# Kernel tuning notes

Measured on AMD Instinct MI355X. Metric: run time of the kernel, lower is better.

The kernel has to match this reference:

```python
import jax, jax.numpy as jnp
import numpy as np

B, CIN, H, W = 16, 256, 56, 56
D, HEADS, KS, PAD, STRIDE, M = 256, 8, 3, 1, 1, 4
K = KS * KS
N = D // HEADS
# relative_indices: sum of window coords, flattened row-major, values in [0, 2*KS-2]
REL = (np.arange(KS)[:, None] + np.arange(KS)[None, :]).reshape(-1)


def setup_inputs() -> dict:
    key = jax.random.key(0)
    ks = jax.random.split(key, 7)
    return {
        "x": jax.random.normal(ks[0], (B, CIN, H, W), jnp.float32),
        "q": jax.random.normal(ks[1], (B, D, 1), jnp.float32),
        "Wk": jax.random.normal(ks[2], (D, CIN), jnp.float32) * 0.05,
        "Wv": jax.random.normal(ks[3], (D, CIN), jnp.float32) * 0.05,
        "pos_emb": jax.random.normal(ks[4], (1, 2 * KS - 1), jnp.float32),
        "Wlin": jax.random.normal(ks[5], (1, M), jnp.float32),
        "Wproj": jax.random.normal(ks[6], (D, D), jnp.float32) * 0.05,
    }


def _unfold(t):
    # torch nn.Unfold: (B,C,H,W) -> (B, C*K, L); patches feature dim ordered (C, kh, kw)
    p = jax.lax.conv_general_dilated_patches(
        t, (KS, KS), (STRIDE, STRIDE), [(PAD, PAD), (PAD, PAD)])
    b, _, ho, wo = p.shape
    return p.reshape(b, -1, ho * wo), ho, wo


def reference(x, q, Wk, Wv, pos_emb, Wlin, Wproj):
    b = x.shape[0]
    k = jnp.einsum('oc,bchw->bohw', Wk, x)  # 1x1 conv, no bias
    v = jnp.einsum('oc,bchw->bohw', Wv, x)
    ku, ho, wo = _unfold(k)
    vu, _, _ = _unfold(v)
    L = ho * wo
    ku = ku.reshape(b, HEADS, N, K, L)  # (b, h, n, k, l)
    vu = vu.reshape(b, HEADS, N, K, L)
    qh = q.reshape(b, HEADS, N)  # learned per-batch query, d=1 squeezed
    attn = jnp.einsum('bhn,bhnkl->bhlk', qh, ku)  # (b,h,l,K)
    attn = attn + pos_emb[0, REL]  # relative position bias, shape (K,)
    attn = jax.nn.softmax(attn, axis=-1)
    # repeat d(=1) -> m identical rows then Linear(m,1,no bias): equals scale by sum(Wlin)
    attn = attn * jnp.sum(Wlin)
    out = jnp.einsum('bhlk,bhnkl->bhnl', attn, vu)  # (b,h,n,l)
    out = out.reshape(b, D, ho, wo)  # fold with kernel 1 == reshape
    return jnp.einsum('oc,bchw->bohw', Wproj, out)  # 1x1 proj conv
```

## Files before the change

### kernel.cpp

```cpp
#include <hip/hip_runtime.h>

#define B_     16
#define D_     256
#define HEADS_ 8
#define N_     32
#define H_     56
#define W_     56
#define L_     3136
#define LDB    40
#define LDX    66

typedef short short8 __attribute__((ext_vector_type(8)));
typedef float f32x4  __attribute__((ext_vector_type(4)));

__device__ __forceinline__ unsigned short f2bf(float f) {
    union { float f; unsigned u; } c; c.f = f;
    unsigned u = c.u;
    u += 0x7fffu + ((u >> 16) & 1u);
    return (unsigned short)(u >> 16);
}

__global__ __launch_bounds__(256) void convert_w_kernel(
    const float* __restrict__ w0, const float* __restrict__ w1,
    const float* __restrict__ w2, unsigned short* __restrict__ o0,
    unsigned short* __restrict__ o1, unsigned short* __restrict__ o2)
{
    const float* src; unsigned short* dst;
    if (blockIdx.y == 0)      { src = w0; dst = o0; }
    else if (blockIdx.y == 1) { src = w1; dst = o1; }
    else                      { src = w2; dst = o2; }
    const int i = (blockIdx.x * 256 + threadIdx.x) * 4;
    float4 v = *(const float4*)(src + i);
    uint2 o;
    o.x = (unsigned)f2bf(v.x) | ((unsigned)f2bf(v.y) << 16);
    o.y = (unsigned)f2bf(v.z) | ((unsigned)f2bf(v.w) << 16);
    *(uint2*)(dst + i) = o;
}

__global__ __launch_bounds__(256, 2) void gemm_kv_mfma(
    const float* __restrict__ x, const unsigned short* __restrict__ Wkb,
    const unsigned short* __restrict__ Wvb, const float* __restrict__ q,
    unsigned short* __restrict__ Vo, float* __restrict__ S)
{
    __shared__ float Xs[32][LDX];

    const int bb = blockIdx.z;
    const int l0 = blockIdx.x * 64;
    const int t  = threadIdx.x;
    const int w    = t >> 6;
    const int lane = t & 63;
    const int col  = lane & 15;
    const int quad = lane >> 4;

    f32x4 accK[4][4], accV[4][4];
#pragma unroll
    for (int mi = 0; mi < 4; ++mi)
#pragma unroll
        for (int ni = 0; ni < 4; ++ni) {
            accK[mi][ni] = (f32x4){0.f, 0.f, 0.f, 0.f};
            accV[mi][ni] = (f32x4){0.f, 0.f, 0.f, 0.f};
        }

    const int xc = t >> 3;
    const int xl = (t & 7) * 8;
    const float* xrow = x + ((size_t)bb * D_ + xc) * L_ + l0 + xl;

    const unsigned short* wk0 = Wkb + (size_t)(w * 64 + col) * D_ + quad * 8;
    const unsigned short* wv0 = Wvb + (size_t)(w * 64 + col) * D_ + quad * 8;

    for (int kt = 0; kt < 8; ++kt) {
        const int c0 = kt * 32;
        const float* xp = xrow + (size_t)c0 * L_;
        float4 x0 = *(const float4*)xp;
        float4 x1 = *(const float4*)(xp + 4);
        short8 ak[4], av[4];
#pragma unroll
        for (int mi = 0; mi < 4; ++mi) {
            ak[mi] = *(const short8*)(wk0 + (size_t)mi * 16 * D_ + c0);
            av[mi] = *(const short8*)(wv0 + (size_t)mi * 16 * D_ + c0);
        }

        __syncthreads();
        *(float2*)&Xs[xc][xl + 0] = make_float2(x0.x, x0.y);
        *(float2*)&Xs[xc][xl + 2] = make_float2(x0.z, x0.w);
        *(float2*)&Xs[xc][xl + 4] = make_float2(x1.x, x1.y);
        *(float2*)&Xs[xc][xl + 6] = make_float2(x1.z, x1.w);
        __syncthreads();

        short8 bfr[4];
#pragma unroll
        for (int ni = 0; ni < 4; ++ni)
#pragma unroll
            for (int j = 0; j < 8; ++j)
                bfr[ni][j] = (short)f2bf(Xs[quad * 8 + j][ni * 16 + col]);

#pragma unroll
        for (int mi = 0; mi < 4; ++mi)
#pragma unroll
            for (int ni = 0; ni < 4; ++ni) {
                accK[mi][ni] = __builtin_amdgcn_mfma_f32_16x16x32_bf16(ak[mi], bfr[ni], accK[mi][ni], 0, 0, 0);
                accV[mi][ni] = __builtin_amdgcn_mfma_f32_16x16x32_bf16(av[mi], bfr[ni], accV[mi][ni], 0, 0, 0);
            }
    }

#pragma unroll
    for (int mi = 0; mi < 4; ++mi) {
        const int hh = w * 2 + (mi >> 1);
        const int dn = (mi & 1) * 16 + quad * 4;
#pragma unroll
        for (int ni = 0; ni < 4; ++ni) {
            unsigned short pk[4];
#pragma unroll
            for (int r = 0; r < 4; ++r) pk[r] = f2bf(accV[mi][ni][r]);
            const int l = l0 + ni * 16 + col;
            *(uint2*)(Vo + ((((size_t)(bb * HEADS_ + hh)) * L_ + l) << 5) + dn) =
                *(const uint2*)pk;
        }
    }

    float qv[4][4];
#pragma unroll
    for (int mi = 0; mi < 4; ++mi)
#pragma unroll
        for (int r = 0; r < 4; ++r)
            qv[mi][r] = q[bb * D_ + w * 64 + mi * 16 + quad * 4 + r];

#pragma unroll
    for (int ni = 0; ni < 4; ++ni) {
        float s0 = 0.f, s1 = 0.f;
#pragma unroll
        for (int r = 0; r < 4; ++r) {
            s0 = fmaf(qv[0][r], accK[0][ni][r], s0);
            s0 = fmaf(qv[1][r], accK[1][ni][r], s0);
            s1 = fmaf(qv[2][r], accK[2][ni][r], s1);
            s1 = fmaf(qv[3][r], accK[3][ni][r], s1);
        }
        s0 += __shfl_xor(s0, 16, 64);
        s0 += __shfl_xor(s0, 32, 64);
        s1 += __shfl_xor(s1, 16, 64);
        s1 += __shfl_xor(s1, 32, 64);
        if (lane < 16) {
            const int l = l0 + ni * 16 + col;
            S[(size_t)(bb * HEADS_ + w * 2) * L_ + l]     = s0;
            S[(size_t)(bb * HEADS_ + w * 2 + 1) * L_ + l] = s1;
        }
    }
}

__global__ __launch_bounds__(256) void attend_kernel(
    const float* __restrict__ S, const unsigned short* __restrict__ Vo,
    const float* __restrict__ pos_emb, const float* __restrict__ Wlin,
    unsigned short* __restrict__ Om)
{
    __shared__ unsigned short Vs[10][58][8];
    __shared__ float Ss[10][58];

    const int band = blockIdx.x;
    const int half = blockIdx.y;
    const int bh   = blockIdx.z;
    const int y0   = band * 8;
    const int t    = threadIdx.x;

    const float* Sb = S + (size_t)bh * L_;
    for (int j = t; j < 580; j += 256) {
        const int row = j / 58, c = j - row * 58;
        const int gr = y0 - 1 + row, gc = c - 1;
        const bool in = (gr >= 0 && gr < H_ && gc >= 0 && gc < W_);
        Ss[row][c] = in ? Sb[gr * W_ + gc] : 0.f;
        uint4 vv = make_uint4(0u, 0u, 0u, 0u);
        if (in)
            vv = *(const uint4*)(Vo + (((size_t)bh * L_ + gr * W_ + gc) << 5) + half * 8);
        *(uint4*)&Vs[row][c][0] = vv;
    }
    __syncthreads();

    const float scale = Wlin[0] + Wlin[1] + Wlin[2] + Wlin[3];
    const float pe0 = pos_emb[0], pe1 = pos_emb[1], pe2 = pos_emb[2];
    const float pe3 = pos_emb[3], pe4 = pos_emb[4];
    const float bias[9] = {pe0, pe1, pe2, pe1, pe2, pe3, pe2, pe3, pe4};

    for (int p = t; p < 448; p += 256) {
        const int yl = p / 56, xx = p - yl * 56;
        const int lr = yl + 1, lc = xx + 1;

        float lg[9], m = -1e30f;
#pragma unroll
        for (int dy = 0; dy < 3; ++dy)
#pragma unroll
            for (int dx = 0; dx < 3; ++dx) {
                const int k = dy * 3 + dx;
                lg[k] = Ss[lr - 1 + dy][lc - 1 + dx] + bias[k];
                m = fmaxf(m, lg[k]);
            }
        float ssum = 0.f;
#pragma unroll
        for (int k = 0; k < 9; ++k) { lg[k] = __expf(lg[k] - m); ssum += lg[k]; }
        const float inv = scale / ssum;

        float om[8] = {0.f, 0.f, 0.f, 0.f, 0.f, 0.f, 0.f, 0.f};
#pragma unroll
        for (int dy = 0; dy < 3; ++dy)
#pragma unroll
            for (int dx = 0; dx < 3; ++dx) {
                const float wk = lg[dy * 3 + dx] * inv;
                const uint4 v = *(const uint4*)&Vs[lr - 1 + dy][lc - 1 + dx][0];
                const unsigned* u = (const unsigned*)&v;
#pragma unroll
                for (int i = 0; i < 4; ++i) {
                    union { unsigned uu; float f; } lo, hi;
                    lo.uu = u[i] << 16;
                    hi.uu = u[i] & 0xffff0000u;
                    om[2 * i]     = fmaf(wk, lo.f, om[2 * i]);
                    om[2 * i + 1] = fmaf(wk, hi.f, om[2 * i + 1]);
                }
            }

        unsigned short ob[8];
#pragma unroll
        for (int i = 0; i < 8; ++i) ob[i] = f2bf(om[i]);
        const int l = (y0 + yl) * W_ + xx;
        *(uint4*)(Om + (((size_t)bh * L_ + l) << 5) + half * 8) = *(const uint4*)ob;
    }
}

__global__ __launch_bounds__(256, 2) void gemm_proj_mfma(
    const unsigned short* __restrict__ Om, const unsigned short* __restrict__ Wpb,
    float* __restrict__ Out)
{
    __shared__ unsigned short Bs[64][LDB];

    const int bb = blockIdx.z;
    const int l0 = blockIdx.x * 64;
    const int t  = threadIdx.x;
    const int w    = t >> 6;
    const int lane = t & 63;
    const int col  = lane & 15;
    const int quad = lane >> 4;

    f32x4 acc[4][4];
#pragma unroll
    for (int mi = 0; mi < 4; ++mi)
#pragma unroll
        for (int ni = 0; ni < 4; ++ni) acc[mi][ni] = (f32x4){0.f, 0.f, 0.f, 0.f};

    const int srow = t >> 2;
    const int skc  = (t & 3) * 8;
    const unsigned short* wp0 = Wpb + (size_t)(w * 64 + col) * D_ + quad * 8;

    for (int kt = 0; kt < 8; ++kt) {
        const int c0 = kt * 32;
        uint4 bg = *(const uint4*)(Om +
            ((((size_t)(bb * HEADS_ + kt)) * L_ + l0 + srow) << 5) + skc);
        short8 a[4];
#pragma unroll
        for (int mi = 0; mi < 4; ++mi)
            a[mi] = *(const short8*)(wp0 + (size_t)mi * 16 * D_ + c0);

        __syncthreads();
        *(uint4*)&Bs[srow][skc] = bg;
        __syncthreads();

        short8 bfr[4];
#pragma unroll
        for (int ni = 0; ni < 4; ++ni)
            bfr[ni] = *(const short8*)&Bs[ni * 16 + col][quad * 8];

#pragma unroll
        for (int mi = 0; mi < 4; ++mi)
#pragma unroll
            for (int ni = 0; ni < 4; ++ni)
                acc[mi][ni] = __builtin_amdgcn_mfma_f32_16x16x32_bf16(a[mi], bfr[ni], acc[mi][ni], 0, 0, 0);
    }

#pragma unroll
    for (int mi = 0; mi < 4; ++mi)
#pragma unroll
        for (int ni = 0; ni < 4; ++ni)
#pragma unroll
            for (int r = 0; r < 4; ++r) {
                const int d = w * 64 + mi * 16 + quad * 4 + r;
                const int l = l0 + ni * 16 + col;
                Out[((size_t)bb * D_ + d) * L_ + l] = acc[mi][ni][r];
            }
}

extern "C" void kernel_launch(void* const* d_in, const int* in_sizes, int n_in,
                              void* d_out, int out_size, void* d_ws, size_t ws_size,
                              hipStream_t stream)
{
    const float* x       = (const float*)d_in[0];
    const float* q       = (const float*)d_in[1];
    const float* Wk      = (const float*)d_in[2];
    const float* Wv      = (const float*)d_in[3];
    const float* pos_emb = (const float*)d_in[4];
    const float* Wlin    = (const float*)d_in[5];
    const float* Wproj   = (const float*)d_in[6];
    float* out = (float*)d_out;

    const size_t planeE = (size_t)B_ * D_ * L_;
    unsigned short* Vo  = (unsigned short*)d_ws;
    unsigned short* Om  = Vo + planeE;
    unsigned short* Wkb = Om + planeE;
    unsigned short* Wvb = Wkb + D_ * D_;
    unsigned short* Wpb = Wvb + D_ * D_;
    float*          S   = (float*)(Wpb + D_ * D_);

    convert_w_kernel<<<dim3(64, 3), 256, 0, stream>>>(Wk, Wv, Wproj, Wkb, Wvb, Wpb);
    gemm_kv_mfma<<<dim3(L_ / 64, 1, B_), 256, 0, stream>>>(x, Wkb, Wvb, q, Vo, S);
    attend_kernel<<<dim3(7, 4, B_ * HEADS_), 256, 0, stream>>>(
        S, Vo, pos_emb, Wlin, Om);
    gemm_proj_mfma<<<dim3(L_ / 64, 1, B_), 256, 0, stream>>>(Om, Wpb, out);
}
```

Measured before the change: 195.7 us.

## Fold q into Wk, split GEMMs over output halves, double-buffer LDS tiles

Precomputes qk = q·Wk per batch and head, so the K projection shrinks from a full 256-row GEMM to a single 16-row MFMA tile (8 live heads, zero-padded) that directly yields the attention scores. The K/V and proj GEMMs now split the 256 output rows across two blocks, doubling grid size and halving accumulators per block. x is converted to bf16 once per element on the store to LDS instead of once per fragment read, and the next k-tile's global loads are prefetched into registers with a double-buffered LDS tile. The cost is that x tiles are loaded twice (once per half), plus an extra small kernel launch, and qk is rounded to bf16, which changes precision slightly.

```diff
diff --git a/kernel.cpp b/kernel.cpp
--- a/kernel.cpp
+++ b/kernel.cpp
@@ -8,7 +8,6 @@
 #define W_     56
 #define L_     3136
 #define LDB    40
-#define LDX    66
 
 typedef short short8 __attribute__((ext_vector_type(8)));
 typedef float f32x4  __attribute__((ext_vector_type(4)));
@@ -20,15 +19,27 @@
     return (unsigned short)(u >> 16);
 }
 
+__global__ __launch_bounds__(256) void qk_kernel(
+    const float* __restrict__ q, const float* __restrict__ Wk,
+    unsigned short* __restrict__ qkb)
+{
+    const int h = blockIdx.x;
+    const int b = blockIdx.y;
+    const int c = threadIdx.x;
+    float s = 0.f;
+#pragma unroll
+    for (int n = 0; n < 32; ++n)
+        s = fmaf(q[b * D_ + h * 32 + n], Wk[(size_t)(h * 32 + n) * D_ + c], s);
+    qkb[((size_t)b * 16 + h) * D_ + c]     = f2bf(s);
+    qkb[((size_t)b * 16 + 8 + h) * D_ + c] = 0;
+}
+
 __global__ __launch_bounds__(256) void convert_w_kernel(
     const float* __restrict__ w0, const float* __restrict__ w1,
-    const float* __restrict__ w2, unsigned short* __restrict__ o0,
-    unsigned short* __restrict__ o1, unsigned short* __restrict__ o2)
-{
-    const float* src; unsigned short* dst;
-    if (blockIdx.y == 0)      { src = w0; dst = o0; }
-    else if (blockIdx.y == 1) { src = w1; dst = o1; }
-    else                      { src = w2; dst = o2; }
+    unsigned short* __restrict__ o0, unsigned short* __restrict__ o1)
+{
+    const float* src = blockIdx.y ? w1 : w0;
+    unsigned short* dst = blockIdx.y ? o1 : o0;
     const int i = (blockIdx.x * 256 + threadIdx.x) * 4;
     float4 v = *(const float4*)(src + i);
     uint2 o;
@@ -37,76 +48,86 @@
     *(uint2*)(dst + i) = o;
 }
 
-__global__ __launch_bounds__(256, 2) void gemm_kv_mfma(
-    const float* __restrict__ x, const unsigned short* __restrict__ Wkb,
-    const unsigned short* __restrict__ Wvb, const float* __restrict__ q,
+__global__ __launch_bounds__(256) void gemm_kv_mfma(
+    const float* __restrict__ x, const unsigned short* __restrict__ Wvb,
+    const unsigned short* __restrict__ qkb,
     unsigned short* __restrict__ Vo, float* __restrict__ S)
 {
-    __shared__ float Xs[32][LDX];
-
-    const int bb = blockIdx.z;
-    const int l0 = blockIdx.x * 64;
-    const int t  = threadIdx.x;
+    __shared__ unsigned short Bs[2][64][LDB];
+
+    const int bb  = blockIdx.z;
+    const int bx  = blockIdx.x;
+    const int l0  = (bx >> 1) * 64;
+    const int fam = bx & 1;
+    const int d0  = fam * 128;
+    const int t   = threadIdx.x;
     const int w    = t >> 6;
     const int lane = t & 63;
     const int col  = lane & 15;
     const int quad = lane >> 4;
 
-    f32x4 accK[4][4], accV[4][4];
-#pragma unroll
-    for (int mi = 0; mi < 4; ++mi)
-#pragma unroll
-        for (int ni = 0; ni < 4; ++ni) {
-            accK[mi][ni] = (f32x4){0.f, 0.f, 0.f, 0.f};
-            accV[mi][ni] = (f32x4){0.f, 0.f, 0.f, 0.f};
+    f32x4 accV[2][4];
+    f32x4 accS = (f32x4){0.f, 0.f, 0.f, 0.f};
+#pragma unroll
+    for (int mi = 0; mi < 2; ++mi)
+#pragma unroll
+        for (int ni = 0; ni < 4; ++ni) accV[mi][ni] = (f32x4){0.f, 0.f, 0.f, 0.f};
+
+    const int sc  = t >> 3;
+    const int sl8 = (t & 7) * 8;
+    const float* xrow = x + ((size_t)bb * D_ + sc) * L_ + l0 + sl8;
+    const unsigned short* wv0 = Wvb + (size_t)(d0 + w * 32 + col) * D_ + quad * 8;
+    const unsigned short* qk0 = qkb + ((size_t)bb * 16 + col) * D_ + quad * 8;
+
+    float4 xa = *(const float4*)xrow;
+    float4 xb4 = *(const float4*)(xrow + 4);
+    short8 av[2], aq;
+    av[0] = *(const short8*)wv0;
+    av[1] = *(const short8*)(wv0 + 16 * D_);
+    aq    = *(const short8*)qk0;
+
+    for (int kt = 0; kt < 8; ++kt) {
+        const int buf = kt & 1;
+        unsigned short hb[8];
+        hb[0] = f2bf(xa.x);  hb[1] = f2bf(xa.y);
+        hb[2] = f2bf(xa.z);  hb[3] = f2bf(xa.w);
+        hb[4] = f2bf(xb4.x); hb[5] = f2bf(xb4.y);
+        hb[6] = f2bf(xb4.z); hb[7] = f2bf(xb4.w);
+#pragma unroll
+        for (int i = 0; i < 8; ++i) Bs[buf][sl8 + i][sc] = hb[i];
+        __syncthreads();
+
+        float4 xan, xbn; short8 avn[2], aqn;
+        if (kt < 7) {
+            const float* xp = xrow + (size_t)(kt + 1) * 32 * L_;
+            xan = *(const float4*)xp;
+            xbn = *(const float4*)(xp + 4);
+            avn[0] = *(const short8*)(wv0 + (kt + 1) * 32);
+            avn[1] = *(const short8*)(wv0 + 16 * D_ + (kt + 1) * 32);
+            aqn    = *(const short8*)(qk0 + (kt + 1) * 32);
         }
 
-    const int xc = t >> 3;
-    const int xl = (t & 7) * 8;
-    const float* xrow = x + ((size_t)bb * D_ + xc) * L_ + l0 + xl;
-
-    const unsigned short* wk0 = Wkb + (size_t)(w * 64 + col) * D_ + quad * 8;
-    const unsigned short* wv0 = Wvb + (size_t)(w * 64 + col) * D_ + quad * 8;
-
-    for (int kt = 0; kt < 8; ++kt) {
-        const int c0 = kt * 32;
-        const float* xp = xrow + (size_t)c0 * L_;
-        float4 x0 = *(const float4*)xp;
-        float4 x1 = *(const float4*)(xp + 4);
-        short8 ak[4], av[4];
-#pragma unroll
-        for (int mi = 0; mi < 4; ++mi) {
-            ak[mi] = *(const short8*)(wk0 + (size_t)mi * 16 * D_ + c0);
-            av[mi] = *(const short8*)(wv0 + (size_t)mi * 16 * D_ + c0);
-        }
-
-        __syncthreads();
-        *(float2*)&Xs[xc][xl + 0] = make_float2(x0.x, x0.y);
-        *(float2*)&Xs[xc][xl + 2] = make_float2(x0.z, x0.w);
-        *(float2*)&Xs[xc][xl + 4] = make_float2(x1.x, x1.y);
-        *(float2*)&Xs[xc][xl + 6] = make_float2(x1.z, x1.w);
-        __syncthreads();
-
         short8 bfr[4];
 #pragma unroll
         for (int ni = 0; ni < 4; ++ni)
-#pragma unroll
-            for (int j = 0; j < 8; ++j)
-                bfr[ni][j] = (short)f2bf(Xs[quad * 8 + j][ni * 16 + col]);
-
-#pragma unroll
-        for (int mi = 0; mi < 4; ++mi)
-#pragma unroll
-            for (int ni = 0; ni < 4; ++ni) {
-                accK[mi][ni] = __builtin_amdgcn_mfma_f32_16x16x32_bf16(ak[mi], bfr[ni], accK[mi][ni], 0, 0, 0);
-                accV[mi][ni] = __builtin_amdgcn_mfma_f32_16x16x32_bf16(av[mi], bfr[ni], accV[mi][ni], 0, 0, 0);
-            }
-    }
-
-#pragma unroll
-    for (int mi = 0; mi < 4; ++mi) {
-        const int hh = w * 2 + (mi >> 1);
-        const int dn = (mi & 1) * 16 + quad * 4;
+            bfr[ni] = *(const short8*)&Bs[buf][ni * 16 + col][quad * 8];
+
+#pragma unroll
+        for (int mi = 0; mi < 2; ++mi)
+#pragma unroll
+            for (int ni = 0; ni < 4; ++ni)
+                accV[mi][ni] = __builtin_amdgcn_mfma_f32_16x16x32_bf16(
+                    av[mi], bfr[ni], accV[mi][ni], 0, 0, 0);
+        if (fam == 0)
+            accS = __builtin_amdgcn_mfma_f32_16x16x32_bf16(aq, bfr[w], accS, 0, 0, 0);
+
+        xa = xan; xb4 = xbn; av[0] = avn[0]; av[1] = avn[1]; aq = aqn;
+    }
+
+    const int hh = fam * 4 + w;
+#pragma unroll
+    for (int mi = 0; mi < 2; ++mi) {
+        const int dn = mi * 16 + quad * 4;
 #pragma unroll
         for (int ni = 0; ni < 4; ++ni) {
             unsigned short pk[4];
@@ -118,31 +139,12 @@
         }
     }
 
-    float qv[4][4];
-#pragma unroll
-    for (int mi = 0; mi < 4; ++mi)
-#pragma unroll
-        for (int r = 0; r < 4; ++r)
-            qv[mi][r] = q[bb * D_ + w * 64 + mi * 16 + quad * 4 + r];
-
-#pragma unroll
-    for (int ni = 0; ni < 4; ++ni) {
-        float s0 = 0.f, s1 = 0.f;
+    if (fam == 0 && quad < 2) {
+        const int l = l0 + w * 16 + col;
 #pragma unroll
         for (int r = 0; r < 4; ++r) {
-            s0 = fmaf(qv[0][r], accK[0][ni][r], s0);
-            s0 = fmaf(qv[1][r], accK[1][ni][r], s0);
-            s1 = fmaf(qv[2][r], accK[2][ni][r], s1);
-            s1 = fmaf(qv[3][r], accK[3][ni][r], s1);
-        }
-        s0 += __shfl_xor(s0, 16, 64);
-        s0 += __shfl_xor(s0, 32, 64);
-        s1 += __shfl_xor(s1, 16, 64);
-        s1 += __shfl_xor(s1, 32, 64);
-        if (lane < 16) {
-            const int l = l0 + ni * 16 + col;
-            S[(size_t)(bb * HEADS_ + w * 2) * L_ + l]     = s0;
-            S[(size_t)(bb * HEADS_ + w * 2 + 1) * L_ + l] = s1;
+            const int h = quad * 4 + r;
+            S[(size_t)(bb * HEADS_ + h) * L_ + l] = accS[r];
         }
     }
 }
@@ -223,62 +225,73 @@
     }
 }
 
-__global__ __launch_bounds__(256, 2) void gemm_proj_mfma(
+__global__ __launch_bounds__(256) void gemm_proj_mfma(
     const unsigned short* __restrict__ Om, const unsigned short* __restrict__ Wpb,
     float* __restrict__ Out)
 {
-    __shared__ unsigned short Bs[64][LDB];
-
-    const int bb = blockIdx.z;
-    const int l0 = blockIdx.x * 64;
-    const int t  = threadIdx.x;
+    __shared__ unsigned short Bs[2][64][LDB];
+
+    const int bb  = blockIdx.z;
+    const int bx  = blockIdx.x;
+    const int l0  = (bx >> 1) * 64;
+    const int fam = bx & 1;
+    const int d0  = fam * 128;
+    const int t   = threadIdx.x;
     const int w    = t >> 6;
     const int lane = t & 63;
     const int col  = lane & 15;
     const int quad = lane >> 4;
 
-    f32x4 acc[4][4];
-#pragma unroll
-    for (int mi = 0; mi < 4; ++mi)
+    f32x4 acc[2][4];
+#pragma unroll
+    for (int mi = 0; mi < 2; ++mi)
 #pragma unroll
         for (int ni = 0; ni < 4; ++ni) acc[mi][ni] = (f32x4){0.f, 0.f, 0.f, 0.f};
 
     const int srow = t >> 2;
     const int skc  = (t & 3) * 8;
-    const unsigned short* wp0 = Wpb + (size_t)(w * 64 + col) * D_ + quad * 8;
+    const unsigned short* omr = Om + (((size_t)bb * HEADS_ * L_ + l0 + srow) << 5) + skc;
+    const unsigned short* wp0 = Wpb + (size_t)(d0 + w * 32 + col) * D_ + quad * 8;
+
+    uint4 bg = *(const uint4*)omr;
+    short8 a[2];
+    a[0] = *(const short8*)wp0;
+    a[1] = *(const short8*)(wp0 + 16 * D_);
 
     for (int kt = 0; kt < 8; ++kt) {
-        const int c0 = kt * 32;
-        uint4 bg = *(const uint4*)(Om +
-            ((((size_t)(bb * HEADS_ + kt)) * L_ + l0 + srow) << 5) + skc);
-        short8 a[4];
-#pragma unroll
-        for (int mi = 0; mi < 4; ++mi)
-            a[mi] = *(const short8*)(wp0 + (size_t)mi * 16 * D_ + c0);
-
+        const int buf = kt & 1;
+        *(uint4*)&Bs[buf][srow][skc] = bg;
         __syncthreads();
-        *(uint4*)&Bs[srow][skc] = bg;
-        __syncthreads();
+
+        uint4 bgn; short8 an[2];
+        if (kt < 7) {
+            bgn = *(const uint4*)(omr + (((size_t)(kt + 1)) * L_ << 5));
+            an[0] = *(const short8*)(wp0 + (kt + 1) * 32);
+            an[1] = *(const short8*)(wp0 + 16 * D_ + (kt + 1) * 32);
+        }
 
         short8 bfr[4];
 #pragma unroll
         for (int ni = 0; ni < 4; ++ni)
-            bfr[ni] = *(const short8*)&Bs[ni * 16 + col][quad * 8];
-
-#pragma unroll
-        for (int mi = 0; mi < 4; ++mi)
+            bfr[ni] = *(const short8*)&Bs[buf][ni * 16 + col][quad * 8];
+
+#pragma unroll
+        for (int mi = 0; mi < 2; ++mi)
 #pragma unroll
             for (int ni = 0; ni < 4; ++ni)
-                acc[mi][ni] = __builtin_amdgcn_mfma_f32_16x16x32_bf16(a[mi], bfr[ni], acc[mi][ni], 0, 0, 0);
-    }
-
-#pragma unroll
-    for (int mi = 0; mi < 4; ++mi)
+                acc[mi][ni] = __builtin_amdgcn_mfma_f32_16x16x32_bf16(
+                    a[mi], bfr[ni], acc[mi][ni], 0, 0, 0);
+
+        bg = bgn; a[0] = an[0]; a[1] = an[1];
+    }
+
+#pragma unroll
+    for (int mi = 0; mi < 2; ++mi)
 #pragma unroll
         for (int ni = 0; ni < 4; ++ni)
 #pragma unroll
             for (int r = 0; r < 4; ++r) {
-                const int d = w * 64 + mi * 16 + quad * 4 + r;
+                const int d = d0 + w * 32 + mi * 16 + quad * 4 + r;
                 const int l = l0 + ni * 16 + col;
                 Out[((size_t)bb * D_ + d) * L_ + l] = acc[mi][ni][r];
             }
@@ -300,14 +313,15 @@
     const size_t planeE = (size_t)B_ * D_ * L_;
     unsigned short* Vo  = (unsigned short*)d_ws;
     unsigned short* Om  = Vo + planeE;
-    unsigned short* Wkb = Om + planeE;
-    unsigned short* Wvb = Wkb + D_ * D_;
+    unsigned short* Wvb = Om + planeE;
     unsigned short* Wpb = Wvb + D_ * D_;
-    float*          S   = (float*)(Wpb + D_ * D_);
-
-    convert_w_kernel<<<dim3(64, 3), 256, 0, stream>>>(Wk, Wv, Wproj, Wkb, Wvb, Wpb);
-    gemm_kv_mfma<<<dim3(L_ / 64, 1, B_), 256, 0, stream>>>(x, Wkb, Wvb, q, Vo, S);
+    unsigned short* qkb = Wpb + D_ * D_;
+    float*          S   = (float*)(qkb + B_ * 16 * D_);
+
+    qk_kernel<<<dim3(HEADS_, B_), 256, 0, stream>>>(q, Wk, qkb);
+    convert_w_kernel<<<dim3(64, 2), 256, 0, stream>>>(Wv, Wproj, Wvb, Wpb);
+    gemm_kv_mfma<<<dim3(2 * (L_ / 64), 1, B_), 256, 0, stream>>>(x, Wvb, qkb, Vo, S);
     attend_kernel<<<dim3(7, 4, B_ * HEADS_), 256, 0, stream>>>(
         S, Vo, pos_emb, Wlin, Om);
-    gemm_proj_mfma<<<dim3(L_ / 64, 1, B_), 256, 0, stream>>>(Om, Wpb, out);
-}
+    gemm_proj_mfma<<<dim3(2 * (L_ / 64), 1, B_), 256, 0, stream>>>(Om, Wpb, out);
+}
```

Measured after the change: 225.0 us. +15.0%, slower.
